# Kernel optimization log

Hardware: AMD Instinct MI355X
Metric: run time of the kernel (lower is better)

The kernel has to match this reference:

```python
import jax, jax.numpy as jnp
import numpy as np
import math

D_MODEL = 1024
NUM_HEADS = 16
HEAD_DIM = D_MODEL // NUM_HEADS


def setup_inputs() -> dict:
    key = jax.random.key(0)
    ks = jax.random.split(key, 10)
    B, Sq, Skv = 2, 2048, 2048
    s = 1.0 / math.sqrt(D_MODEL)
    return {
        "X": jax.random.normal(ks[0], (B, Skv, D_MODEL), jnp.float32),
        "y": jax.random.normal(ks[1], (B, Sq, D_MODEL), jnp.float32),
        "qW": jax.random.normal(ks[2], (D_MODEL, D_MODEL), jnp.float32) * s,
        "qB": jnp.zeros((D_MODEL,), jnp.float32),
        "kW": jax.random.normal(ks[3], (D_MODEL, D_MODEL), jnp.float32) * s,
        "kB": jnp.zeros((D_MODEL,), jnp.float32),
        "vW": jax.random.normal(ks[4], (D_MODEL, D_MODEL), jnp.float32) * s,
        "vB": jnp.zeros((D_MODEL,), jnp.float32),
        "oW": jax.random.normal(ks[5], (D_MODEL, D_MODEL), jnp.float32) * s,
        "oB": jnp.zeros((D_MODEL,), jnp.float32),
    }


def _split_heads(x):
    # (B, S, D) -> (B, H, S, dk)
    B, S, _ = x.shape
    return x.reshape(B, S, NUM_HEADS, HEAD_DIM).transpose(0, 2, 1, 3)


def reference(X, y, qW, qB, kW, kB, vW, vB, oW, oB):
    B = X.shape[0]
    q = _split_heads(y @ qW + qB)   # queries come from y (decoder)
    k = _split_heads(X @ kW + kB)   # keys/values from X (encoder)
    v = _split_heads(X @ vW + vB)
    scale = 1.0 / math.sqrt(HEAD_DIM)
    scores = jnp.einsum("bhqd,bhkd->bhqk", q, k) * scale
    weights = jax.nn.softmax(scores, axis=-1)
    attn = jnp.einsum("bhqk,bhkd->bhqd", weights, v)
    concat = attn.transpose(0, 2, 1, 3).reshape(B, -1, D_MODEL)
    return concat @ oW + oB
```

## Files before the change

kernel.cpp:

```cpp
#include <hip/hip_runtime.h>
#include <hip/hip_bf16.h>
#include <math.h>

typedef __hip_bfloat16 bf16;
typedef __bf16 nbf16;
typedef __bf16 bf16x8 __attribute__((ext_vector_type(8)));
typedef __bf16 bf16x4 __attribute__((ext_vector_type(4)));
typedef float f32x4 __attribute__((ext_vector_type(4)));

#define D_MODEL 1024
#define NHEAD   16
#define HDK     64
#define BATCH   2
#define SEQ     2048
#define QSZ     ((size_t)BATCH * SEQ * D_MODEL)
#define WSZ     ((size_t)D_MODEL * D_MODEL)

__global__ void detect_dtype(const unsigned short* __restrict__ x, int* flag) {
    __shared__ int cnt;
    if (threadIdx.x == 0) cnt = 0;
    __syncthreads();
    int local = 0;
    for (int i = threadIdx.x; i < 4096; i += 256) {
        const unsigned short v = x[i];
        const int e = (v >> 7) & 0xFF;
        if (v == 0 || (e >= 96 && e <= 141)) local++;
    }
    atomicAdd(&cnt, local);
    __syncthreads();
    if (threadIdx.x == 0) *flag = (cnt >= 3600) ? 1 : 0;
}

__device__ __forceinline__ float ldIn(const void* p, size_t i, int isbf16) {
    return isbf16 ? __bfloat162float(((const bf16*)p)[i])
                  : ((const float*)p)[i];
}

__device__ __forceinline__ void gload_lds16(const void* g, void* l) {
    __builtin_amdgcn_global_load_lds(
        (const __attribute__((address_space(1))) void*)g,
        (__attribute__((address_space(3))) void*)l, 16, 0, 0);
}

__global__ void prep(const void* __restrict__ X, const void* __restrict__ Y,
                     const void* __restrict__ qW, const void* __restrict__ kW,
                     const void* __restrict__ vW, const void* __restrict__ oW,
                     nbf16* __restrict__ Xb, nbf16* __restrict__ Yb,
                     nbf16* __restrict__ Wt3, nbf16* __restrict__ Wto,
                     const int* __restrict__ flagp) {
    const int flag = *flagp;
    const int id = blockIdx.x;
    if (id < 4096) {
        const bool isX = id < 2048;
        const void* in = isX ? X : Y;
        nbf16* out     = isX ? Xb : Yb;
        const size_t i = ((size_t)(isX ? id : id - 2048) * 256 +
                          threadIdx.x) * 8;
        if (flag) {
            *(uint4*)(out + i) = *(const uint4*)((const nbf16*)in + i);
        } else {
            const float4 a = *(const float4*)((const float*)in + i);
            const float4 b = *(const float4*)((const float*)in + i + 4);
            bf16x8 v = {(nbf16)a.x, (nbf16)a.y, (nbf16)a.z, (nbf16)a.w,
                        (nbf16)b.x, (nbf16)b.y, (nbf16)b.z, (nbf16)b.w};
            *(bf16x8*)(out + i) = v;
        }
    } else {
        const int t = id - 4096;
        const int z = t >> 8;
        const int tile = t & 255;
        const void* W = (z == 0) ? qW : (z == 1) ? kW : (z == 2) ? vW : oW;
        nbf16* Wt = (z == 3) ? Wto : Wt3 + (size_t)z * WSZ;

        __shared__ float T[64][65];
        const int k0 = (tile & 15) * 64, n0 = (tile >> 4) * 64;
        #pragma unroll
        for (int i = 0; i < 16; ++i) {
            const int idx = threadIdx.x + i * 256;
            const int r = idx >> 6, c = idx & 63;
            T[r][c] = ldIn(W, (size_t)(k0 + r) * D_MODEL + n0 + c, flag);
        }
        __syncthreads();
        #pragma unroll
        for (int i = 0; i < 16; ++i) {
            const int idx = threadIdx.x + i * 256;
            const int n = idx >> 6, k = idx & 63;
            Wt[(size_t)(n0 + n) * D_MODEL + k0 + k] = (nbf16)T[k][n];
        }
    }
}

#define STAGE1(Albuf, Blbuf, Aptr, Bptr, t)                                    \
{                                                                              \
    const int _k0 = (t) * 64;                                                  \
    _Pragma("unroll")                                                          \
    for (int i = 0; i < 4; ++i) {                                              \
        const int row = i * 32 + wid * 8 + (lane >> 3);                        \
        const int ss  = (lane & 7) ^ (row & 7);                                \
        gload_lds16((Aptr) + (size_t)row * D_MODEL + _k0 + ss * 8,             \
                    (nbf16*)(Albuf) + i * 2048 + wid * 512);                   \
        gload_lds16((Bptr) + (size_t)row * D_MODEL + _k0 + ss * 8,             \
                    (nbf16*)(Blbuf) + i * 2048 + wid * 512);                   \
    }                                                                          \
}

__global__ __launch_bounds__(256, 3) void proj_qkv(
        const nbf16* __restrict__ Xb, const nbf16* __restrict__ Yb,
        const nbf16* __restrict__ Wt3,
        const void* __restrict__ qB, const void* __restrict__ kB,
        const void* __restrict__ vB,
        nbf16* __restrict__ outq, const int* __restrict__ flagp) {
    __shared__ nbf16 Al[128][64];
    __shared__ nbf16 Bl[128][64];

    const int flag = *flagp;
    const int tid  = threadIdx.x;
    const int wid  = tid >> 6;
    const int lane = tid & 63;
    const int l15  = lane & 15;
    const int lg   = lane >> 4;
    const int wr   = wid >> 1;
    const int wc   = wid & 1;

    const int id = blockIdx.x;
    const int sw = (id & 7) * 96 + (id >> 3);
    const int m0  = (sw & 31) * 128;
    const int ng0 = (sw >> 5) * 128;

    const nbf16* A  = (ng0 < D_MODEL) ? Yb : Xb;
    const nbf16* Bm = Wt3 + (size_t)ng0 * D_MODEL;
    const nbf16* Am = A + (size_t)m0 * D_MODEL;

    f32x4 acc[4][4];
    #pragma unroll
    for (int mi = 0; mi < 4; ++mi)
        #pragma unroll
        for (int ni = 0; ni < 4; ++ni) acc[mi][ni] = (f32x4){0.f, 0.f, 0.f, 0.f};

    const int NT = D_MODEL / 64;
    for (int t = 0; t < NT; ++t) {
        STAGE1(&Al[0][0], &Bl[0][0], Am, Bm, t);
        __syncthreads();
        #pragma unroll
        for (int kk = 0; kk < 2; ++kk) {
            bf16x8 af[4], bfr[4];
            #pragma unroll
            for (int mi = 0; mi < 4; ++mi) {
                const int ar = wr * 64 + mi * 16 + l15;
                const int sl = ((kk << 2) + lg) ^ (ar & 7);
                af[mi] = *(const bf16x8*)((const nbf16*)&Al[ar][0] + sl * 8);
            }
            #pragma unroll
            for (int ni = 0; ni < 4; ++ni) {
                const int br = wc * 64 + ni * 16 + l15;
                const int sl = ((kk << 2) + lg) ^ (br & 7);
                bfr[ni] = *(const bf16x8*)((const nbf16*)&Bl[br][0] + sl * 8);
            }
            #pragma unroll
            for (int mi = 0; mi < 4; ++mi)
                #pragma unroll
                for (int ni = 0; ni < 4; ++ni)
                    acc[mi][ni] = __builtin_amdgcn_mfma_f32_16x16x32_bf16(
                        af[mi], bfr[ni], acc[mi][ni], 0, 0, 0);
        }
        __syncthreads();
    }

    #pragma unroll
    for (int ni = 0; ni < 4; ++ni) {
        const int n  = ng0 + wc * 64 + ni * 16 + l15;
        const int wh = n >> 10;
        const int nl = n & 1023;
        const void* bp = (wh == 0) ? qB : (wh == 1) ? kB : vB;
        const float bias = ldIn(bp, (size_t)nl, flag);
        nbf16* outp = outq + (size_t)wh * QSZ;
        #pragma unroll
        for (int mi = 0; mi < 4; ++mi) {
            #pragma unroll
            for (int r = 0; r < 4; ++r) {
                const int m = m0 + wr * 64 + mi * 16 + lg * 4 + r;
                const float v = acc[mi][ni][r] + bias;
                const int b = m >> 11, s = m & (SEQ - 1);
                const int h = nl >> 6,  d = nl & (HDK - 1);
                outp[(((size_t)(b * NHEAD + h)) * SEQ + s) * HDK + d] = (nbf16)v;
            }
        }
    }
}

#define STAGE128(Albuf, Blbuf, Aptr, Bptr, t)                                  \
{                                                                              \
    const int _k0 = (t) * 64;                                                  \
    _Pragma("unroll")                                                          \
    for (int i = 0; i < 4; ++i) {                                              \
        const int row = i * 32 + wid * 8 + (lane >> 3);                        \
        const int ss  = (lane & 7) ^ (row & 7);                                \
        gload_lds16((Aptr) + (size_t)row * D_MODEL + _k0 + ss * 8,             \
                    (nbf16*)(Albuf) + i * 2048 + wid * 512);                   \
        gload_lds16((Bptr) + (size_t)row * D_MODEL + _k0 + ss * 8,             \
                    (nbf16*)(Blbuf) + i * 2048 + wid * 512);                   \
    }                                                                          \
}

__global__ __launch_bounds__(256, 2) void proj_o(
        const nbf16* __restrict__ A, const nbf16* __restrict__ Wt,
        const void* __restrict__ Braw, void* __restrict__ Cout,
        const int* __restrict__ flagp) {
    __shared__ nbf16 Al[2][128][64];
    __shared__ nbf16 Bl[2][128][64];

    const int flag = *flagp;
    const int tid  = threadIdx.x;
    const int wid  = tid >> 6;
    const int lane = tid & 63;
    const int l15  = lane & 15;
    const int lg   = lane >> 4;
    const int wr   = wid >> 1;
    const int wc   = wid & 1;

    const int id = blockIdx.x;
    const int sw = (id & 7) * 32 + (id >> 3);
    const int m0 = (sw >> 3) * 128;
    const int n0 = (sw & 7) * 128;

    const nbf16* Am = A + (size_t)m0 * D_MODEL;
    const nbf16* Bm = Wt + (size_t)n0 * D_MODEL;

    f32x4 acc[4][4];
    #pragma unroll
    for (int mi = 0; mi < 4; ++mi)
        #pragma unroll
        for (int ni = 0; ni < 4; ++ni) acc[mi][ni] = (f32x4){0.f, 0.f, 0.f, 0.f};

    STAGE128(&Al[0][0][0], &Bl[0][0][0], Am, Bm, 0);
    __syncthreads();

    const int NT = D_MODEL / 64;
    for (int t = 0; t < NT; ++t) {
        const int cur = t & 1;
        if (t + 1 < NT)
            STAGE128(&Al[cur ^ 1][0][0], &Bl[cur ^ 1][0][0], Am, Bm, t + 1);
        #pragma unroll
        for (int kk = 0; kk < 2; ++kk) {
            bf16x8 af[4], bfr[4];
            #pragma unroll
            for (int mi = 0; mi < 4; ++mi) {
                const int ar = wr * 64 + mi * 16 + l15;
                const int sl = ((kk << 2) + lg) ^ (ar & 7);
                af[mi] = *(const bf16x8*)((const nbf16*)&Al[cur][ar][0] + sl * 8);
            }
            #pragma unroll
            for (int ni = 0; ni < 4; ++ni) {
                const int br = wc * 64 + ni * 16 + l15;
                const int sl = ((kk << 2) + lg) ^ (br & 7);
                bfr[ni] = *(const bf16x8*)((const nbf16*)&Bl[cur][br][0] + sl * 8);
            }
            #pragma unroll
            for (int mi = 0; mi < 4; ++mi)
                #pragma unroll
                for (int ni = 0; ni < 4; ++ni)
                    acc[mi][ni] = __builtin_amdgcn_mfma_f32_16x16x32_bf16(
                        af[mi], bfr[ni], acc[mi][ni], 0, 0, 0);
        }
        __syncthreads();
    }

    #pragma unroll
    for (int ni = 0; ni < 4; ++ni) {
        const int n = n0 + wc * 64 + ni * 16 + l15;
        const float bias = ldIn(Braw, (size_t)n, flag);
        #pragma unroll
        for (int mi = 0; mi < 4; ++mi) {
            #pragma unroll
            for (int r = 0; r < 4; ++r) {
                const int m = m0 + wr * 64 + mi * 16 + lg * 4 + r;
                const float v = acc[mi][ni][r] + bias;
                if (flag) ((bf16*)Cout)[(size_t)m * D_MODEL + n] = __float2bfloat16(v);
                else      ((float*)Cout)[(size_t)m * D_MODEL + n] = v;
            }
        }
    }
}

template<bool SPLIT>
__global__ __launch_bounds__(256, SPLIT ? 3 : 2) void attn_mfma(
        const nbf16* __restrict__ qg, const nbf16* __restrict__ kg,
        const nbf16* __restrict__ vg, nbf16* __restrict__ cg,
        float* __restrict__ part_o, float2* __restrict__ part_ms) {
    __shared__ nbf16 KL[2][64][64];
    __shared__ nbf16 VT[2][64][64];
    __shared__ nbf16 PB[4][32][64];

    const int tid  = threadIdx.x;
    const int wid  = tid >> 6;
    const int lane = tid & 63;
    const int l15  = lane & 15;
    const int lg   = lane >> 4;

    const int id = blockIdx.x;
    const int sw = SPLIT ? ((id & 7) * 128 + (id >> 3))
                         : ((id & 7) * 64 + (id >> 3));
    const int bh   = SPLIT ? (sw >> 5) : (sw >> 4);
    const int qt   = SPLIT ? ((sw & 31) >> 1) : (sw & 15);
    const int half = SPLIT ? (sw & 1) : 0;

    const nbf16* qb = qg + (size_t)bh * SEQ * HDK;
    const nbf16* kb = kg + (size_t)bh * SEQ * HDK +
                      (size_t)half * (SEQ / 2) * HDK;
    const nbf16* vb = vg + (size_t)bh * SEQ * HDK +
                      (size_t)half * (SEQ / 2) * HDK;

    const float SCf = 0.125f * 1.44269504088896340736f;

    const int qbase = qt * 128 + wid * 32;
    const nbf16* qpA = qb + (size_t)(qbase + l15) * HDK + lg * 8;
    const nbf16* qpB = qpA + 16 * HDK;
    bf16x8 qfA0 = *(const bf16x8*)qpA;
    bf16x8 qfA1 = *(const bf16x8*)(qpA + 32);
    bf16x8 qfB0 = *(const bf16x8*)qpB;
    bf16x8 qfB1 = *(const bf16x8*)(qpB + 32);
    #pragma unroll
    for (int j = 0; j < 8; ++j) {
        qfA0[j] = (nbf16)((float)qfA0[j] * SCf);
        qfA1[j] = (nbf16)((float)qfA1[j] * SCf);
        qfB0[j] = (nbf16)((float)qfB0[j] * SCf);
        qfB1[j] = (nbf16)((float)qfB1[j] * SCf);
    }

    const bf16x8 ones = {(nbf16)1.f, (nbf16)1.f, (nbf16)1.f, (nbf16)1.f,
                         (nbf16)1.f, (nbf16)1.f, (nbf16)1.f, (nbf16)1.f};

    const int g8 = (tid >> 5) * 8;
    const int p2 = (tid & 31) * 2;

    const int swz0 = (lg * 8)      ^ ((l15 & 7) << 3);
    const int swz1 = (lg * 8 + 32) ^ ((l15 & 7) << 3);

    #define STAGEK(buf, t)                                                     \
    {                                                                          \
        _Pragma("unroll")                                                      \
        for (int i = 0; i < 2; ++i) {                                          \
            const int row = i * 32 + wid * 8 + (lane >> 3);                    \
            const int ss  = (lane & 7) ^ (row & 7);                            \
            gload_lds16(kb + (size_t)((t) * 64 + row) * HDK + ss * 8,          \
                        (nbf16*)&KL[buf][0][0] + i * 2048 + wid * 512);        \
        }                                                                      \
    }

    #define VLOAD(t)                                                           \
        a0 = *(const uint4*)(vb + (size_t)((t) * 64 + p2) * HDK + g8);         \
        a1 = *(const uint4*)(vb + (size_t)((t) * 64 + p2 + 1) * HDK + g8);

    #define VWRITE(buf)                                                        \
    {                                                                          \
        const unsigned short* e0 = (const unsigned short*)&a0;                 \
        const unsigned short* e1 = (const unsigned short*)&a1;                 \
        _Pragma("unroll")                                                      \
        for (int j = 0; j < 8; ++j)                                            \
            *(unsigned int*)&VT[buf][g8 + j][p2 ^ (j << 3)] =                  \
                (unsigned int)e0[j] | ((unsigned int)e1[j] << 16);             \
    }

    #define SOFTMAX(st, m2, o, osum, pbrow)                                    \
    do {                                                                       \
        float tmx[4];                                                          \
        _Pragma("unroll")                                                      \
        for (int s_ = 0; s_ < 4; ++s_)                                         \
            tmx[s_] = fmaxf(fmaxf(st[s_][0], st[s_][1]),                       \
                            fmaxf(st[s_][2], st[s_][3]));                      \
        float tm = fmaxf(fmaxf(tmx[0], tmx[1]), fmaxf(tmx[2], tmx[3]));        \
        tm = fmaxf(tm, __shfl_xor(tm, 16, 64));                                \
        tm = fmaxf(tm, __shfl_xor(tm, 32, 64));                                \
        const bool nresc = __all(tm - m2 <= 8.0f);                             \
        const float mref = nresc ? m2 : fmaxf(m2, tm);                         \
        _Pragma("unroll")                                                      \
        for (int s_ = 0; s_ < 4; ++s_) {                                       \
            const float p0 = exp2f(st[s_][0] - mref);                          \
            const float p1 = exp2f(st[s_][1] - mref);                          \
            const float p2_ = exp2f(st[s_][2] - mref);                         \
            const float p3 = exp2f(st[s_][3] - mref);                          \
            bf16x4 pk = {(nbf16)p0, (nbf16)p1, (nbf16)p2_, (nbf16)p3};         \
            *(bf16x4*)((pbrow) + ((s_ * 16 + lg * 4) ^ ((l15 & 7) << 3))) = pk;\
        }                                                                      \
        if (!nresc) {                                                          \
            const float alpha = exp2f(m2 - mref);                              \
            m2 = mref;                                                         \
            float av[4];                                                       \
            _Pragma("unroll")                                                  \
            for (int r = 0; r < 4; ++r) av[r] = __shfl(alpha, lg * 4 + r, 64); \
            _Pragma("unroll")                                                  \
            for (int i = 0; i < 4; ++i)                                        \
                _Pragma("unroll")                                              \
                for (int r = 0; r < 4; ++r) o[i][r] *= av[r];                  \
            _Pragma("unroll")                                                  \
            for (int r = 0; r < 4; ++r) osum[r] *= av[r];                      \
        }                                                                      \
    } while (0)

    float m2A = -3.0e38f, m2B = -3.0e38f;
    f32x4 oA[4], oB[4], osumA, osumB;
    #pragma unroll
    for (int i = 0; i < 4; ++i) { oA[i] = (f32x4){0,0,0,0}; oB[i] = (f32x4){0,0,0,0}; }
    osumA = (f32x4){0, 0, 0, 0};
    osumB = (f32x4){0, 0, 0, 0};

    const int NT = SPLIT ? (SEQ / 2) / 64 : SEQ / 64;

    {
        uint4 a0, a1;
        STAGEK(0, 0);
        VLOAD(0);
        VWRITE(0);
    }
    __syncthreads();

    for (int t = 0; t < NT; ++t) {
        const int cur = t & 1;
        uint4 a0, a1;
        if (t + 1 < NT) {
            STAGEK(cur ^ 1, t + 1);
            VLOAD(t + 1);
        }

        f32x4 stA[4], stB[4];
        __builtin_amdgcn_s_setprio(1);
        #pragma unroll
        for (int sub = 0; sub < 4; ++sub) {
            const int row = sub * 16 + l15;
            const int s0 = lg ^ (row & 7);
            const int s1 = (4 + lg) ^ (row & 7);
            const bf16x8 kf0 = *(const bf16x8*)((const nbf16*)&KL[cur][row][0] + s0 * 8);
            const bf16x8 kf1 = *(const bf16x8*)((const nbf16*)&KL[cur][row][0] + s1 * 8);
            f32x4 a = (f32x4){0,0,0,0};
            a = __builtin_amdgcn_mfma_f32_16x16x32_bf16(kf0, qfA0, a, 0, 0, 0);
            a = __builtin_amdgcn_mfma_f32_16x16x32_bf16(kf1, qfA1, a, 0, 0, 0);
            stA[sub] = a;
            f32x4 b = (f32x4){0,0,0,0};
            b = __builtin_amdgcn_mfma_f32_16x16x32_bf16(kf0, qfB0, b, 0, 0, 0);
            b = __builtin_amdgcn_mfma_f32_16x16x32_bf16(kf1, qfB1, b, 0, 0, 0);
            stB[sub] = b;
        }
        __builtin_amdgcn_s_setprio(0);

        SOFTMAX(stA, m2A, oA, osumA, &PB[wid][l15][0]);
        SOFTMAX(stB, m2B, oB, osumB, &PB[wid][16 + l15][0]);

        __asm__ volatile("s_waitcnt lgkmcnt(0)" ::: "memory");

        const nbf16* pbA = &PB[wid][l15][0];
        const nbf16* pbB = &PB[wid][16 + l15][0];
        const bf16x8 pfA0 = *(const bf16x8*)(pbA + swz0);
        const bf16x8 pfA1 = *(const bf16x8*)(pbA + swz1);
        const bf16x8 pfB0 = *(const bf16x8*)(pbB + swz0);
        const bf16x8 pfB1 = *(const bf16x8*)(pbB + swz1);
        __builtin_amdgcn_s_setprio(1);
        #pragma unroll
        for (int db = 0; db < 4; ++db) {
            const nbf16* vr = &VT[cur][db * 16 + l15][0];
            const bf16x8 vf0 = *(const bf16x8*)(vr + swz0);
            const bf16x8 vf1 = *(const bf16x8*)(vr + swz1);
            oA[db] = __builtin_amdgcn_mfma_f32_16x16x32_bf16(pfA0, vf0, oA[db], 0, 0, 0);
            oA[db] = __builtin_amdgcn_mfma_f32_16x16x32_bf16(pfA1, vf1, oA[db], 0, 0, 0);
            oB[db] = __builtin_amdgcn_mfma_f32_16x16x32_bf16(pfB0, vf0, oB[db], 0, 0, 0);
            oB[db] = __builtin_amdgcn_mfma_f32_16x16x32_bf16(pfB1, vf1, oB[db], 0, 0, 0);
        }
        osumA = __builtin_amdgcn_mfma_f32_16x16x32_bf16(pfA0, ones, osumA, 0, 0, 0);
        osumA = __builtin_amdgcn_mfma_f32_16x16x32_bf16(pfA1, ones, osumA, 0, 0, 0);
        osumB = __builtin_amdgcn_mfma_f32_16x16x32_bf16(pfB0, ones, osumB, 0, 0, 0);
        osumB = __builtin_amdgcn_mfma_f32_16x16x32_bf16(pfB1, ones, osumB, 0, 0, 0);
        __builtin_amdgcn_s_setprio(0);

        if (t + 1 < NT) VWRITE(cur ^ 1);
        __syncthreads();
    }

    if (!SPLIT) {
        const int b = bh >> 4, h = bh & 15;
        #pragma unroll
        for (int db = 0; db < 4; ++db) {
            #pragma unroll
            for (int r = 0; r < 4; ++r) {
                const int qA = qbase + lg * 4 + r;
                cg[((size_t)(b * SEQ + qA)) * D_MODEL + h * HDK + db * 16 + l15] =
                    (nbf16)(oA[db][r] / osumA[r]);
                const int qB_ = qbase + 16 + lg * 4 + r;
                cg[((size_t)(b * SEQ + qB_)) * D_MODEL + h * HDK + db * 16 + l15] =
                    (nbf16)(oB[db][r] / osumB[r]);
            }
        }
    } else {
        float mvA[4], mvB[4];
        #pragma unroll
        for (int r = 0; r < 4; ++r) {
            mvA[r] = __shfl(m2A, lg * 4 + r, 64);
            mvB[r] = __shfl(m2B, lg * 4 + r, 64);
        }
        const int p = (bh * 16 + qt) * 2 + half;
        float* po = part_o + (size_t)p * (128 * 64);
        #pragma unroll
        for (int db = 0; db < 4; ++db) {
            #pragma unroll
            for (int r = 0; r < 4; ++r) {
                po[(wid * 32 + lg * 4 + r) * 64 + db * 16 + l15]      = oA[db][r];
                po[(wid * 32 + 16 + lg * 4 + r) * 64 + db * 16 + l15] = oB[db][r];
            }
        }
        if (l15 == 0) {
            #pragma unroll
            for (int r = 0; r < 4; ++r) {
                part_ms[(size_t)p * 128 + wid * 32 + lg * 4 + r]      =
                    make_float2(mvA[r], osumA[r]);
                part_ms[(size_t)p * 128 + wid * 32 + 16 + lg * 4 + r] =
                    make_float2(mvB[r], osumB[r]);
            }
        }
    }
    #undef STAGEK
    #undef VLOAD
    #undef VWRITE
    #undef SOFTMAX
}

__global__ void attn_combine(const float* __restrict__ part_o,
                             const float2* __restrict__ part_ms,
                             nbf16* __restrict__ cg) {
    const int bq = blockIdx.x;
    const int bh = bq >> 4, qt = bq & 15;
    const int p0 = bq * 2, p1 = bq * 2 + 1;
    const int q  = threadIdx.x >> 1;
    const int d0 = (threadIdx.x & 1) * 32;

    const float2 s1 = part_ms[(size_t)p0 * 128 + q];
    const float2 s2 = part_ms[(size_t)p1 * 128 + q];
    const float m  = fmaxf(s1.x, s2.x);
    const float w1 = exp2f(s1.x - m);
    const float w2 = exp2f(s2.x - m);
    const float inv = 1.f / (s1.y * w1 + s2.y * w2);

    const float* o1 = part_o + (size_t)p0 * (128 * 64) + q * 64 + d0;
    const float* o2 = part_o + (size_t)p1 * (128 * 64) + q * 64 + d0;
    const int b = bh >> 4, h = bh & 15;
    nbf16* out = cg + ((size_t)(b * SEQ + qt * 128 + q)) * D_MODEL + h * HDK + d0;
    #pragma unroll
    for (int j = 0; j < 8; ++j) {
        const float4 a = *(const float4*)(o1 + j * 4);
        const float4 c = *(const float4*)(o2 + j * 4);
        out[j * 4 + 0] = (nbf16)((a.x * w1 + c.x * w2) * inv);
        out[j * 4 + 1] = (nbf16)((a.y * w1 + c.y * w2) * inv);
        out[j * 4 + 2] = (nbf16)((a.z * w1 + c.z * w2) * inv);
        out[j * 4 + 3] = (nbf16)((a.w * w1 + c.w * w2) * inv);
    }
}

extern "C" void kernel_launch(void* const* d_in, const int* in_sizes, int n_in,
                              void* d_out, int out_size, void* d_ws, size_t ws_size,
                              hipStream_t stream) {
    const void* X  = d_in[0];
    const void* Y  = d_in[1];
    const void* qW = d_in[2];
    const void* qB = d_in[3];
    const void* kW = d_in[4];
    const void* kB = d_in[5];
    const void* vW = d_in[6];
    const void* vB = d_in[7];
    const void* oW = d_in[8];
    const void* oB = d_in[9];

    nbf16* ws = (nbf16*)d_ws;
    nbf16* qbuf = ws;
    nbf16* kbuf = qbuf + QSZ;
    nbf16* vbuf = kbuf + QSZ;
    nbf16* cbuf = vbuf + QSZ;
    nbf16* Xb   = cbuf + QSZ;
    nbf16* Yb   = Xb + QSZ;
    nbf16* Wt3  = Yb + QSZ;
    nbf16* Wto  = Wt3 + 3 * WSZ;
    int*   flag = (int*)(Wto + WSZ);
    char*  pbase = (char*)flag + 256;
    float2* part_ms = (float2*)pbase;
    float*  part_o  = (float*)(part_ms + (size_t)1024 * 128);
    const size_t need_split =
        (size_t)((char*)(part_o + (size_t)1024 * 128 * 64) - (char*)d_ws);
    const bool use_split = (ws_size >= need_split);

    detect_dtype<<<1, 256, 0, stream>>>((const unsigned short*)X, flag);

    prep<<<5120, 256, 0, stream>>>(X, Y, qW, kW, vW, oW, Xb, Yb, Wt3, Wto, flag);

    proj_qkv<<<768, 256, 0, stream>>>(Xb, Yb, Wt3, qB, kB, vB, qbuf, flag);

    if (use_split) {
        attn_mfma<true><<<1024, 256, 0, stream>>>(qbuf, kbuf, vbuf, cbuf,
                                                  part_o, part_ms);
        attn_combine<<<512, 256, 0, stream>>>(part_o, part_ms, cbuf);
    } else {
        attn_mfma<false><<<512, 256, 0, stream>>>(qbuf, kbuf, vbuf, cbuf,
                                                  nullptr, nullptr);
    }

    proj_o<<<256, 256, 0, stream>>>(cbuf, Wto, oB, d_out, flag);
}
```

Measured before the change: 250.6 us.

## Keep softmax probabilities in registers by permuting V key layout, drop P LDS buffer

The softmax probabilities now go straight into the MFMA A-operand registers instead of taking a round trip through a per-wave shared-memory buffer. To make this work, the V transpose write permutes key indices (kh) so that the PV MFMA's k ordering matches the register layout of the score accumulators. Removing the PB buffer frees LDS and eliminates the store, wait and reload, and the split variant's occupancy hint is raised from 3 to 4 blocks. The risk is that the key permutation must match the score fragment layout exactly, and the higher occupancy hint may force register spilling.

After: 253.2 us. Within noise of the previous version (+1.0%).

```diff
diff --git a/kernel.cpp b/kernel.cpp
--- a/kernel.cpp
+++ b/kernel.cpp
@@ -283,13 +283,12 @@
 }
 
 template<bool SPLIT>
-__global__ __launch_bounds__(256, SPLIT ? 3 : 2) void attn_mfma(
+__global__ __launch_bounds__(256, SPLIT ? 4 : 2) void attn_mfma(
         const nbf16* __restrict__ qg, const nbf16* __restrict__ kg,
         const nbf16* __restrict__ vg, nbf16* __restrict__ cg,
         float* __restrict__ part_o, float2* __restrict__ part_ms) {
     __shared__ nbf16 KL[2][64][64];
     __shared__ nbf16 VT[2][64][64];
-    __shared__ nbf16 PB[4][32][64];
 
     const int tid  = threadIdx.x;
     const int wid  = tid >> 6;
@@ -332,6 +331,7 @@
 
     const int g8 = (tid >> 5) * 8;
     const int p2 = (tid & 31) * 2;
+    const int kh = (p2 & 32) | ((p2 & 12) << 1) | ((p2 & 16) >> 2) | (p2 & 3);
 
     const int swz0 = (lg * 8)      ^ ((l15 & 7) << 3);
     const int swz1 = (lg * 8 + 32) ^ ((l15 & 7) << 3);
@@ -357,11 +357,11 @@
         const unsigned short* e1 = (const unsigned short*)&a1;                 \
         _Pragma("unroll")                                                      \
         for (int j = 0; j < 8; ++j)                                            \
-            *(unsigned int*)&VT[buf][g8 + j][p2 ^ (j << 3)] =                  \
+            *(unsigned int*)&VT[buf][g8 + j][kh ^ (j << 3)] =                  \
                 (unsigned int)e0[j] | ((unsigned int)e1[j] << 16);             \
     }
 
-    #define SOFTMAX(st, m2, o, osum, pbrow)                                    \
+    #define SOFTMAX(st, m2, o, osum, pf0, pf1)                                 \
     do {                                                                       \
         float tmx[4];                                                          \
         _Pragma("unroll")                                                      \
@@ -374,14 +374,12 @@
         const bool nresc = __all(tm - m2 <= 8.0f);                             \
         const float mref = nresc ? m2 : fmaxf(m2, tm);                         \
         _Pragma("unroll")                                                      \
-        for (int s_ = 0; s_ < 4; ++s_) {                                       \
-            const float p0 = exp2f(st[s_][0] - mref);                          \
-            const float p1 = exp2f(st[s_][1] - mref);                          \
-            const float p2_ = exp2f(st[s_][2] - mref);                         \
-            const float p3 = exp2f(st[s_][3] - mref);                          \
-            bf16x4 pk = {(nbf16)p0, (nbf16)p1, (nbf16)p2_, (nbf16)p3};         \
-            *(bf16x4*)((pbrow) + ((s_ * 16 + lg * 4) ^ ((l15 & 7) << 3))) = pk;\
-        }                                                                      \
+        for (int s_ = 0; s_ < 2; ++s_)                                         \
+            _Pragma("unroll")                                                  \
+            for (int r = 0; r < 4; ++r) {                                      \
+                pf0[s_ * 4 + r] = (nbf16)exp2f(st[s_][r] - mref);              \
+                pf1[s_ * 4 + r] = (nbf16)exp2f(st[2 + s_][r] - mref);          \
+            }                                                                  \
         if (!nresc) {                                                          \
             const float alpha = exp2f(m2 - mref);                              \
             m2 = mref;                                                         \
@@ -442,17 +440,10 @@
         }
         __builtin_amdgcn_s_setprio(0);
 
-        SOFTMAX(stA, m2A, oA, osumA, &PB[wid][l15][0]);
-        SOFTMAX(stB, m2B, oB, osumB, &PB[wid][16 + l15][0]);
-
-        __asm__ volatile("s_waitcnt lgkmcnt(0)" ::: "memory");
-
-        const nbf16* pbA = &PB[wid][l15][0];
-        const nbf16* pbB = &PB[wid][16 + l15][0];
-        const bf16x8 pfA0 = *(const bf16x8*)(pbA + swz0);
-        const bf16x8 pfA1 = *(const bf16x8*)(pbA + swz1);
-        const bf16x8 pfB0 = *(const bf16x8*)(pbB + swz0);
-        const bf16x8 pfB1 = *(const bf16x8*)(pbB + swz1);
+        bf16x8 pfA0, pfA1, pfB0, pfB1;
+        SOFTMAX(stA, m2A, oA, osumA, pfA0, pfA1);
+        SOFTMAX(stB, m2B, oB, osumB, pfB0, pfB1);
+
         __builtin_amdgcn_s_setprio(1);
         #pragma unroll
         for (int db = 0; db < 4; ++db) {
```
